# Performance work log

Hardware: AMD Instinct MI355X
Metric: run time of the kernel (lower is better)

## Reference

```python
import jax, jax.numpy as jnp
import numpy as np

N = 20000          # total atoms
NPG = 40           # atoms per molecule
G = N // NPG       # 500 graphs
DEG = 16           # neighbors per atom
E = N * DEG        # 320000 edges
HID = 128
NF = 128           # num_filters == num Gaussians
CUTOFF = 10.0
L = 3
IN_DIM = 100
LOG2 = 0.6931471805599453


def ssp(x):
    # ShiftedSoftplus: softplus(x) - log(2)
    return jax.nn.softplus(x) - LOG2


def setup_inputs() -> dict:
    key = jax.random.key(0)
    ks = jax.random.split(key, 16)
    rng = np.random.default_rng(0)

    # within-graph random edges, no self loops (mimics radius_graph structure)
    src = np.repeat(np.arange(N), DEG)
    base = (src // NPG) * NPG
    dst = base + (src - base + 1 + rng.integers(0, NPG - 1, size=E)) % NPG
    edge_index = jnp.asarray(np.stack([src, dst]).astype(np.int32))

    box = CUTOFF / np.sqrt(3.0)  # all pairwise distances < cutoff
    pos = jax.random.uniform(ks[0], (N, 3), dtype=jnp.float32) * box
    z = jax.random.randint(ks[1], (N,), 0, IN_DIM, dtype=jnp.int32)
    batch = jnp.asarray((np.arange(N) // NPG).astype(np.int32))

    s = 0.05
    emb = jax.random.normal(ks[2], (IN_DIM, HID), dtype=jnp.float32) * s
    mlp_w1 = jax.random.normal(ks[3], (L, NF, NF), dtype=jnp.float32) * s
    mlp_b1 = jnp.zeros((L, NF), jnp.float32)
    mlp_w2 = jax.random.normal(ks[4], (L, NF, NF), dtype=jnp.float32) * s
    mlp_b2 = jnp.zeros((L, NF), jnp.float32)
    cf_w1 = jax.random.normal(ks[5], (L, HID, NF), dtype=jnp.float32) * s   # no bias
    cf_w2 = jax.random.normal(ks[6], (L, NF, HID), dtype=jnp.float32) * s
    cf_b2 = jnp.zeros((L, HID), jnp.float32)
    lin_w = jax.random.normal(ks[7], (L, HID, HID), dtype=jnp.float32) * s
    lin_b = jnp.zeros((L, HID), jnp.float32)
    head_w1 = jax.random.normal(ks[8], (HID, HID // 2), dtype=jnp.float32) * s
    head_b1 = jnp.zeros((HID // 2,), jnp.float32)
    head_w2 = jax.random.normal(ks[9], (HID // 2, 1), dtype=jnp.float32) * s
    head_b2 = jnp.zeros((1,), jnp.float32)

    return dict(pos=pos, emb=emb, mlp_w1=mlp_w1, mlp_b1=mlp_b1, mlp_w2=mlp_w2,
                mlp_b2=mlp_b2, cf_w1=cf_w1, cf_w2=cf_w2, cf_b2=cf_b2,
                lin_w=lin_w, lin_b=lin_b, head_w1=head_w1, head_b1=head_b1,
                head_w2=head_w2, head_b2=head_b2, z=z, batch=batch,
                edge_index=edge_index)


def reference(pos, emb, mlp_w1, mlp_b1, mlp_w2, mlp_b2, cf_w1, cf_w2, cf_b2,
              lin_w, lin_b, head_w1, head_b1, head_w2, head_b2,
              z, batch, edge_index):
    row, col = edge_index[0], edge_index[1]  # source j, target i (PyG flow)
    d = jnp.linalg.norm(pos[row] - pos[col], axis=-1)  # [E]

    # Gaussian smearing
    offset = jnp.linspace(0.0, CUTOFF, NF)
    coeff = -0.5 / (offset[1] - offset[0]) ** 2
    edge_attr = jnp.exp(coeff * (d[:, None] - offset) ** 2)  # [E, NF]

    # cosine cutoff
    C = 0.5 * (jnp.cos(d * jnp.pi / CUTOFF) + 1.0)  # [E]

    h = emb[z]  # [N, HID]
    for l in range(L):
        # edge filter MLP
        Wf = ssp(edge_attr @ mlp_w1[l] + mlp_b1[l]) @ mlp_w2[l] + mlp_b2[l]
        Wf = Wf * C[:, None]                       # [E, NF]
        x1 = h @ cf_w1[l]                          # [N, NF]
        msg = x1[row] * Wf                         # gather + per-edge filter
        agg = jax.ops.segment_sum(msg, col, num_segments=N)  # scatter-add
        x = ssp(agg @ cf_w2[l] + cf_b2[l])
        x = x @ lin_w[l] + lin_b[l]
        h = h + x

    y = ssp(h @ head_w1 + head_b1) @ head_w2 + head_b2   # [N, 1]
    out = jax.ops.segment_sum(y, batch, num_segments=G).squeeze(-1)  # [G]
    return out
```

## Files before the change

kernel.cpp:

```cpp
#include <hip/hip_runtime.h>
#include <math.h>

#define N_ATOMS 20000
#define G_GRAPHS 500
#define NPG 40
#define DEG 16
#define E_EDGES (N_ATOMS * DEG)
#define EPM (NPG * DEG)
#define HID 128
#define NF 128
#define TBL2 80
#define TROWS (TBL2 + 2)
#define PROWS 81
#define CUTOFF 10.0f
#define LOG2F_ 0.6931471805599453f

typedef __attribute__((ext_vector_type(8))) short short8v;
typedef __attribute__((ext_vector_type(4))) float f32x4;
typedef __attribute__((ext_vector_type(2))) __bf16 bf16x2;
typedef unsigned short ushort_t;

__device__ __forceinline__ float ssp_f(float x) {
  float ax = fabsf(x);
  return fmaxf(x, 0.0f) + log1pf(expf(-ax)) - LOG2F_;
}
__device__ __forceinline__ ushort_t bf16rne(float x) {
  unsigned u = __float_as_uint(x);
  unsigned r = 0x7FFFu + ((u >> 16) & 1u);
  return (ushort_t)((u + r) >> 16);
}
__device__ __forceinline__ unsigned pk2(float a, float b) {
  return (unsigned)bf16rne(a) | ((unsigned)bf16rne(b) << 16);
}
__device__ __forceinline__ float bflo(unsigned u) { return __uint_as_float(u << 16); }
__device__ __forceinline__ float bfhi(unsigned u) { return __uint_as_float(u & 0xFFFF0000u); }
__device__ __forceinline__ int bidx(int row, int col) {
  return row * 128 + (col ^ ((row & 7) << 3));
}
__device__ __forceinline__ float fdot2b(unsigned a, unsigned b, float c) {
#if defined(__has_builtin) && __has_builtin(__builtin_amdgcn_fdot2_f32_bf16)
  return __builtin_amdgcn_fdot2_f32_bf16(__builtin_bit_cast(bf16x2, a),
                                         __builtin_bit_cast(bf16x2, b), c, false);
#else
  return fmaf(bflo(a), bflo(b), fmaf(bfhi(a), bfhi(b), c));
#endif
}

__global__ void k_table(const float* __restrict__ w1_, const float* __restrict__ b1_,
                        const float* __restrict__ w2_, const float* __restrict__ b2_,
                        ushort_t* __restrict__ table_) {
  __shared__ float eaT[NF][8];
  __shared__ float hvT[NF][8];
  int l = blockIdx.y;
  const float* w1 = w1_ + (size_t)l * NF * NF;
  const float* b1 = b1_ + (size_t)l * NF;
  const float* w2 = w2_ + (size_t)l * NF * NF;
  const float* b2 = b2_ + (size_t)l * NF;
  ushort_t* table = table_ + (size_t)l * TROWS * NF;
  int j = threadIdx.x;
  int rbase = blockIdx.x * 8;
  const float hh = CUTOFF / (float)(TBL2 - 1);
  const float delta = CUTOFF / (float)(NF - 1);
  const float coeff = -0.5f / (delta * delta);
#pragma unroll
  for (int rr = 0; rr < 8; ++rr) {
    float d = ((float)(rbase + rr) - 1.0f) * hh;
    float tt = d - delta * (float)j;
    eaT[j][rr] = expf(coeff * tt * tt);
  }
  __syncthreads();
  float acc[8], wreg[16];
  float b1j = b1[j];
#pragma unroll
  for (int rr = 0; rr < 8; ++rr) acc[rr] = b1j;
  for (int kb = 0; kb < NF; kb += 16) {
#pragma unroll
    for (int i = 0; i < 16; ++i) wreg[i] = w1[(kb + i) * NF + j];
#pragma unroll
    for (int i = 0; i < 16; ++i) {
      float4 e0 = *(const float4*)&eaT[kb + i][0];
      float4 e1 = *(const float4*)&eaT[kb + i][4];
      float wv = wreg[i];
      acc[0] = fmaf(e0.x, wv, acc[0]); acc[1] = fmaf(e0.y, wv, acc[1]);
      acc[2] = fmaf(e0.z, wv, acc[2]); acc[3] = fmaf(e0.w, wv, acc[3]);
      acc[4] = fmaf(e1.x, wv, acc[4]); acc[5] = fmaf(e1.y, wv, acc[5]);
      acc[6] = fmaf(e1.z, wv, acc[6]); acc[7] = fmaf(e1.w, wv, acc[7]);
    }
  }
#pragma unroll
  for (int rr = 0; rr < 8; ++rr) hvT[j][rr] = ssp_f(acc[rr]);
  __syncthreads();
  float b2j = b2[j];
#pragma unroll
  for (int rr = 0; rr < 8; ++rr) acc[rr] = b2j;
  for (int kb = 0; kb < NF; kb += 16) {
#pragma unroll
    for (int i = 0; i < 16; ++i) wreg[i] = w2[(kb + i) * NF + j];
#pragma unroll
    for (int i = 0; i < 16; ++i) {
      float4 e0 = *(const float4*)&hvT[kb + i][0];
      float4 e1 = *(const float4*)&hvT[kb + i][4];
      float wv = wreg[i];
      acc[0] = fmaf(e0.x, wv, acc[0]); acc[1] = fmaf(e0.y, wv, acc[1]);
      acc[2] = fmaf(e0.z, wv, acc[2]); acc[3] = fmaf(e0.w, wv, acc[3]);
      acc[4] = fmaf(e1.x, wv, acc[4]); acc[5] = fmaf(e1.y, wv, acc[5]);
      acc[6] = fmaf(e1.z, wv, acc[6]); acc[7] = fmaf(e1.w, wv, acc[7]);
    }
  }
#pragma unroll
  for (int rr = 0; rr < 8; ++rr) {
    int s = rbase + rr;
    if (s < TROWS) {
      float d = ((float)s - 1.0f) * hh;
      float C = 0.5f * (cosf(d * (float)M_PI / CUTOFF) + 1.0f);
      table[(size_t)s * NF + j] = bf16rne(acc[rr] * C);
    }
  }
}

__global__ void k_prep(const float* __restrict__ cf_w1, const float* __restrict__ cf_w2,
                       const float* __restrict__ lin_w, const float* __restrict__ hw1,
                       ushort_t* __restrict__ wtb) {
  __shared__ float tile[32][33];
  int b = blockIdx.x;
  int t = threadIdx.x;
  int tr = t >> 5, tc = t & 31;
  if (b < 36) {
    int m = b >> 2, tj = b & 3;
    int l = m / 3, ty = m % 3;
    const float* src = (ty == 0 ? cf_w1 : ty == 1 ? cf_w2 : lin_w) + (size_t)l * 128 * 128;
    ushort_t* dst = wtb + (size_t)m * 128 * 128;
    for (int ti = 0; ti < 4; ++ti) {
      __syncthreads();
#pragma unroll
      for (int i = 0; i < 4; ++i) {
        int r = tr + i * 8;
        tile[r][tc] = src[(ti * 32 + r) * 128 + tj * 32 + tc];
      }
      __syncthreads();
#pragma unroll
      for (int i = 0; i < 4; ++i) {
        int r = tr + i * 8;
        dst[(tj * 32 + r) * 128 + ti * 32 + tc] = bf16rne(tile[tc][r]);
      }
    }
  } else {
    int tj = b - 36;
    ushort_t* dst = wtb + (size_t)9 * 128 * 128;
    for (int ti = 0; ti < 4; ++ti) {
      __syncthreads();
#pragma unroll
      for (int i = 0; i < 4; ++i) {
        int r = tr + i * 8;
        tile[r][tc] = hw1[(ti * 32 + r) * 64 + tj * 32 + tc];
      }
      __syncthreads();
#pragma unroll
      for (int i = 0; i < 4; ++i) {
        int r = tr + i * 8;
        dst[(tj * 32 + r) * 128 + ti * 32 + tc] = bf16rne(tile[tc][r]);
      }
    }
  }
}

__global__ void __launch_bounds__(512) k_csr(const float* __restrict__ pos,
                                             const int* __restrict__ ei,
                                             uint4* __restrict__ ge,
                                             int* __restrict__ gstart) {
  __shared__ float spos[NPG * 3];
  __shared__ int cnt[NPG];
  __shared__ int pfx[NPG + 1];
  __shared__ uint4 epk[EPM];
  __shared__ unsigned char ecol[EPM];
  __shared__ short ssidx[EPM];
  int g = blockIdx.x, a0 = g * NPG, t = threadIdx.x;
  if (t < NPG * 3) spos[t] = pos[a0 * 3 + t];
  if (t < NPG) cnt[t] = 0;
  __syncthreads();
  int ebase = a0 * DEG;
  const float tscale = (float)(TBL2 - 1) / CUTOFF;
  for (int i = t; i < EPM; i += 512) {
    int r = ei[ebase + i] - a0;
    int c = ei[E_EDGES + ebase + i] - a0;
    float dx = spos[3 * r + 0] - spos[3 * c + 0];
    float dy = spos[3 * r + 1] - spos[3 * c + 1];
    float dz = spos[3 * r + 2] - spos[3 * c + 2];
    float ft = sqrtf(dx * dx + dy * dy + dz * dz) * tscale;
    int i0 = min((int)ft, TBL2 - 2);
    float tt = ft - (float)i0;
    float t2 = tt * tt, t3 = t2 * tt;
    float w0 = 0.5f * (-t3 + 2.f * t2 - tt);
    float w1 = 0.5f * (3.f * t3 - 5.f * t2 + 2.f);
    float w2 = 0.5f * (-3.f * t3 + 4.f * t2 + tt);
    float w3 = 0.5f * (t3 - t2);
    epk[i] = make_uint4(pk2(w0, w1), pk2(w2, w3), (unsigned)(i0 << 7),
                        (unsigned)((r << 6) | (((r & 7) << 2) << 16)));
    ecol[i] = (unsigned char)c;
    atomicAdd(&cnt[c], 1);
  }
  __syncthreads();
  if (t == 0) {
    int s = 0;
    for (int a = 0; a < NPG; ++a) { pfx[a] = s; s += cnt[a]; }
    pfx[NPG] = s;
  }
  __syncthreads();
  int w = t >> 6, lane = t & 63;
  for (int a = w * 5; a < w * 5 + 5; ++a) {
    int p = pfx[a];
#pragma unroll
    for (int ch = 0; ch < EPM / 64; ++ch) {
      int e = ch * 64 + lane;
      bool match = ((int)ecol[e] == a);
      unsigned long long bal = __ballot(match);
      if (match) ssidx[p + __popcll(bal & ((1ull << lane) - 1ull))] = (short)e;
      p += __popcll(bal);
    }
  }
  __syncthreads();
  for (int i = t; i < EPM; i += 512) ge[(size_t)g * EPM + i] = epk[ssidx[i]];
  if (t < NPG) gstart[g * NPG + t] = pfx[t];
}

__global__ void __launch_bounds__(512) k_mol(
    const float* __restrict__ emb, const int* __restrict__ z,
    const uint4* __restrict__ ge, const int* __restrict__ gstart,
    const ushort_t* __restrict__ tblb, const ushort_t* __restrict__ wtb,
    const float* __restrict__ cf_b2, const float* __restrict__ lin_b,
    const float* __restrict__ hb1, const float* __restrict__ hw2,
    const float* __restrict__ hb2, float* __restrict__ out) {
  __shared__ unsigned ptab[PROWS * 128];
  __shared__ ushort_t sb0[48 * 128];
  __shared__ ushort_t sb1[48 * 128];
  __shared__ uint4 sedge[EPM];
  __shared__ int sstart[NPG + 1];
  __shared__ float shead[48];
  __shared__ int sz[NPG];
  int g = blockIdx.x, a0 = g * NPG, t = threadIdx.x;
  int w = t >> 6, l6 = t & 63, r15 = l6 & 15, q = l6 >> 4;
  int colo = w * 16 + r15;
  int half = l6 >> 5, li = l6 & 31, ch0 = li * 4;

  {
    if (t < NPG) sz[t] = z[a0 + t];
    const uint4* gsrc = ge + (size_t)g * EPM;
    for (int i = t; i < EPM; i += 512) sedge[i] = gsrc[i];
    if (t < NPG) sstart[t] = gstart[g * NPG + t];
    if (t == 0) sstart[NPG] = EPM;
    if (t < 48) shead[t] = 0.f;
    ((unsigned*)sb0)[40 * 64 + t] = 0u;
    ((unsigned*)sb1)[40 * 64 + t] = 0u;
    const ushort_t* tg = tblb;
    for (int i = t; i < PROWS * 32; i += 512) {
      int s = i >> 5, c4 = (i & 31) << 2;
      uint2 ar = *(const uint2*)(tg + s * 128 + c4);
      uint2 br = *(const uint2*)(tg + (s + 1) * 128 + c4);
      uint4 o;
      o.x = (ar.x & 0xffffu) | (br.x << 16);
      o.y = (ar.x >> 16) | (br.x & 0xffff0000u);
      o.z = (ar.y & 0xffffu) | (br.y << 16);
      o.w = (ar.y >> 16) | (br.y & 0xffff0000u);
      *(uint4*)&ptab[(s << 7) + c4] = o;
    }
  }
  __syncthreads();

  float hreg[12];
#pragma unroll
  for (int mt = 0; mt < 3; ++mt) {
#pragma unroll
    for (int r = 0; r < 4; ++r) {
      int row = mt * 16 + q * 4 + r;
      float v = 0.f;
      if (row < NPG) {
        v = emb[(size_t)sz[row] * HID + colo];
        sb0[bidx(row, colo)] = bf16rne(v);
      }
      hreg[mt * 4 + r] = v;
    }
  }
  __syncthreads();

  for (int l = 0; l < 3; ++l) {
    const ushort_t* w1t = wtb + (size_t)(l * 3 + 0) * 128 * 128;
    const ushort_t* w2t = wtb + (size_t)(l * 3 + 1) * 128 * 128;
    const ushort_t* lwt = wtb + (size_t)(l * 3 + 2) * 128 * 128;
    if (l > 0) {
      const ushort_t* tg = tblb + (size_t)l * TROWS * 128;
      for (int i = t; i < PROWS * 32; i += 512) {
        int s = i >> 5, c4 = (i & 31) << 2;
        uint2 ar = *(const uint2*)(tg + s * 128 + c4);
        uint2 br = *(const uint2*)(tg + (s + 1) * 128 + c4);
        uint4 o;
        o.x = (ar.x & 0xffffu) | (br.x << 16);
        o.y = (ar.x >> 16) | (br.x & 0xffff0000u);
        o.z = (ar.y & 0xffffu) | (br.y << 16);
        o.w = (ar.y >> 16) | (br.y & 0xffff0000u);
        *(uint4*)&ptab[(s << 7) + c4] = o;
      }
    }
    {
      short8v bfr[4];
      const ushort_t* wp = w1t + (size_t)colo * 128 + q * 8;
#pragma unroll
      for (int ks = 0; ks < 4; ++ks) bfr[ks] = *(const short8v*)(wp + ks * 32);
#pragma unroll
      for (int mt = 0; mt < 3; ++mt) {
        f32x4 acc = (f32x4){0.f, 0.f, 0.f, 0.f};
#pragma unroll
        for (int ks = 0; ks < 4; ++ks) {
          short8v af = *(const short8v*)&sb0[bidx(mt * 16 + r15, ks * 32 + q * 8)];
          acc = __builtin_amdgcn_mfma_f32_16x16x32_bf16(af, bfr[ks], acc, 0, 0, 0);
        }
#pragma unroll
        for (int r = 0; r < 4; ++r) sb1[bidx(mt * 16 + q * 4 + r, colo)] = bf16rne(acc[r]);
      }
    }
    __syncthreads();
    {
      const unsigned* b1u = (const unsigned*)sb1;
      unsigned* b0u = (unsigned*)sb0;
      for (int a = w; a < NPG; a += 8) {
        int kb = sstart[a], ke = sstart[a + 1];
        float a0c = 0.f, a1c = 0.f, a2c = 0.f, a3c = 0.f;
        for (int k = kb; k < ke; k += 2) {
          int idx = k + half;
          uint4 ev = sedge[min(idx, EPM - 1)];
          bool ok = idx < ke;
          unsigned w01 = ok ? ev.x : 0u;
          unsigned w23 = ok ? ev.y : 0u;
          const unsigned* tb = ptab + ev.z + ch0;
          uint4 pa = *(const uint4*)tb;
          uint4 pb = *(const uint4*)(tb + 256);
          uint2 xv = *(const uint2*)&b1u[(ev.w & 0xffffu) + ((li * 2) ^ (ev.w >> 16))];
          float f0 = fdot2b(w01, pa.x, 0.f); f0 = fdot2b(w23, pb.x, f0);
          float f1 = fdot2b(w01, pa.y, 0.f); f1 = fdot2b(w23, pb.y, f1);
          float f2 = fdot2b(w01, pa.z, 0.f); f2 = fdot2b(w23, pb.z, f2);
          float f3 = fdot2b(w01, pa.w, 0.f); f3 = fdot2b(w23, pb.w, f3);
          a0c = fmaf(bflo(xv.x), f0, a0c);
          a1c = fmaf(bfhi(xv.x), f1, a1c);
          a2c = fmaf(bflo(xv.y), f2, a2c);
          a3c = fmaf(bfhi(xv.y), f3, a3c);
        }
        a0c += __shfl_xor(a0c, 32);
        a1c += __shfl_xor(a1c, 32);
        a2c += __shfl_xor(a2c, 32);
        a3c += __shfl_xor(a3c, 32);
        if (half == 0) {
          uint2 o;
          o.x = pk2(a0c, a1c);
          o.y = pk2(a2c, a3c);
          *(uint2*)&b0u[(a << 6) + ((li * 2) ^ ((a & 7) << 2))] = o;
        }
      }
    }
    __syncthreads();
    {
      float bc = cf_b2[(size_t)l * HID + colo];
      short8v bfr[4];
      const ushort_t* wp = w2t + (size_t)colo * 128 + q * 8;
#pragma unroll
      for (int ks = 0; ks < 4; ++ks) bfr[ks] = *(const short8v*)(wp + ks * 32);
#pragma unroll
      for (int mt = 0; mt < 3; ++mt) {
        f32x4 acc = (f32x4){0.f, 0.f, 0.f, 0.f};
#pragma unroll
        for (int ks = 0; ks < 4; ++ks) {
          short8v af = *(const short8v*)&sb0[bidx(mt * 16 + r15, ks * 32 + q * 8)];
          acc = __builtin_amdgcn_mfma_f32_16x16x32_bf16(af, bfr[ks], acc, 0, 0, 0);
        }
#pragma unroll
        for (int r = 0; r < 4; ++r) {
          int row = mt * 16 + q * 4 + r;
          float v = (row < NPG) ? ssp_f(acc[r] + bc) : 0.f;
          sb1[bidx(row, colo)] = bf16rne(v);
        }
      }
    }
    __syncthreads();
    {
      float bc = lin_b[(size_t)l * HID + colo];
      short8v bfr[4];
      const ushort_t* wp = lwt + (size_t)colo * 128 + q * 8;
#pragma unroll
      for (int ks = 0; ks < 4; ++ks) bfr[ks] = *(const short8v*)(wp + ks * 32);
#pragma unroll
      for (int mt = 0; mt < 3; ++mt) {
        f32x4 acc = (f32x4){0.f, 0.f, 0.f, 0.f};
#pragma unroll
        for (int ks = 0; ks < 4; ++ks) {
          short8v af = *(const short8v*)&sb1[bidx(mt * 16 + r15, ks * 32 + q * 8)];
          acc = __builtin_amdgcn_mfma_f32_16x16x32_bf16(af, bfr[ks], acc, 0, 0, 0);
        }
#pragma unroll
        for (int r = 0; r < 4; ++r) {
          int row = mt * 16 + q * 4 + r;
          if (row < NPG) {
            float nh = hreg[mt * 4 + r] + acc[r] + bc;
            hreg[mt * 4 + r] = nh;
            sb0[bidx(row, colo)] = bf16rne(nh);
          }
        }
      }
    }
    __syncthreads();
  }

  {
    const ushort_t* h1t = wtb + (size_t)9 * 128 * 128;
    for (int tile = w; tile < 12; tile += 8) {
      int mt = tile >> 2, nt = tile & 3;
      int col = nt * 16 + r15;
      short8v bfr[4];
      const ushort_t* wp = h1t + (size_t)col * 128 + q * 8;
#pragma unroll
      for (int ks = 0; ks < 4; ++ks) bfr[ks] = *(const short8v*)(wp + ks * 32);
      f32x4 acc = (f32x4){0.f, 0.f, 0.f, 0.f};
#pragma unroll
      for (int ks = 0; ks < 4; ++ks) {
        short8v af = *(const short8v*)&sb0[bidx(mt * 16 + r15, ks * 32 + q * 8)];
        acc = __builtin_amdgcn_mfma_f32_16x16x32_bf16(af, bfr[ks], acc, 0, 0, 0);
      }
      float hb = hb1[col];
      float w2v = hw2[col];
#pragma unroll
      for (int r = 0; r < 4; ++r) {
        int row = mt * 16 + q * 4 + r;
        float y = ssp_f(acc[r] + hb) * w2v;
        y += __shfl_xor(y, 1);
        y += __shfl_xor(y, 2);
        y += __shfl_xor(y, 4);
        y += __shfl_xor(y, 8);
        if (r15 == 0 && row < NPG) atomicAdd(&shead[row], y);
      }
    }
  }
  __syncthreads();
  if (w == 0) {
    float v = (l6 < NPG) ? shead[l6] : 0.f;
#pragma unroll
    for (int off = 32; off; off >>= 1) v += __shfl_xor(v, off);
    if (l6 == 0) out[g] = v + (float)NPG * hb2[0];
  }
}

extern "C" void kernel_launch(void* const* d_in, const int* in_sizes, int n_in,
                              void* d_out, int out_size, void* d_ws, size_t ws_size,
                              hipStream_t stream) {
  const float* pos    = (const float*)d_in[0];
  const float* emb    = (const float*)d_in[1];
  const float* mlp_w1 = (const float*)d_in[2];
  const float* mlp_b1 = (const float*)d_in[3];
  const float* mlp_w2 = (const float*)d_in[4];
  const float* mlp_b2 = (const float*)d_in[5];
  const float* cf_w1  = (const float*)d_in[6];
  const float* cf_w2  = (const float*)d_in[7];
  const float* cf_b2  = (const float*)d_in[8];
  const float* lin_w  = (const float*)d_in[9];
  const float* lin_b  = (const float*)d_in[10];
  const float* hw1    = (const float*)d_in[11];
  const float* hb1    = (const float*)d_in[12];
  const float* hw2    = (const float*)d_in[13];
  const float* hb2    = (const float*)d_in[14];
  const int*   z      = (const int*)d_in[15];
  const int*   ei     = (const int*)d_in[17];

  char* wsb = (char*)d_ws;
  uint4*    ge     = (uint4*)wsb;
  int*      gstart = (int*)(wsb + 5120000);
  ushort_t* tblb   = (ushort_t*)(wsb + 5200000);
  ushort_t* wtb    = (ushort_t*)(wsb + 5262976);
  size_t need = 5262976 + 327680;
  if (ws_size < need) return;

  k_table<<<dim3((TROWS + 7) / 8, 3), NF, 0, stream>>>(mlp_w1, mlp_b1, mlp_w2, mlp_b2, tblb);
  k_prep<<<38, 256, 0, stream>>>(cf_w1, cf_w2, lin_w, hw1, wtb);
  k_csr<<<G_GRAPHS, 512, 0, stream>>>(pos, ei, ge, gstart);
  k_mol<<<G_GRAPHS, 512, 0, stream>>>(emb, z, ge, gstart, tblb, wtb,
                                      cf_b2, lin_b, hb1, hw2, hb2, (float*)d_out);
}
```

Measured before the change: 113.4 us.

## Merge table, weight-prep and CSR kernels into one launch; pre-pair table rows

Fuses the three preprocessing kernels (filter table, weight transpose, per-graph CSR build) into a single launch that dispatches on block index, cutting two kernel launches and their serialization gaps. The filter table is now written in the paired-row layout k_mol consumes, so k_mol copies it into shared memory with plain uint4 loads instead of repacking two rows per layer. Per-atom edge lists are padded to even length with zero-weight edges, which removes the bounds check and select from the inner gather loop. Side effects are slightly more edge storage and idle threads in the table and transpose blocks of the merged launch.

```diff
diff --git a/kernel.cpp b/kernel.cpp
--- a/kernel.cpp
+++ b/kernel.cpp
@@ -7,6 +7,7 @@
 #define DEG 16
 #define E_EDGES (N_ATOMS * DEG)
 #define EPM (NPG * DEG)
+#define EPAD 680
 #define HID 128
 #define NF 128
 #define TBL2 80
@@ -46,194 +47,218 @@
 #endif
 }
 
-__global__ void k_table(const float* __restrict__ w1_, const float* __restrict__ b1_,
-                        const float* __restrict__ w2_, const float* __restrict__ b2_,
-                        ushort_t* __restrict__ table_) {
-  __shared__ float eaT[NF][8];
-  __shared__ float hvT[NF][8];
-  int l = blockIdx.y;
-  const float* w1 = w1_ + (size_t)l * NF * NF;
-  const float* b1 = b1_ + (size_t)l * NF;
-  const float* w2 = w2_ + (size_t)l * NF * NF;
-  const float* b2 = b2_ + (size_t)l * NF;
-  ushort_t* table = table_ + (size_t)l * TROWS * NF;
-  int j = threadIdx.x;
-  int rbase = blockIdx.x * 8;
-  const float hh = CUTOFF / (float)(TBL2 - 1);
-  const float delta = CUTOFF / (float)(NF - 1);
-  const float coeff = -0.5f / (delta * delta);
-#pragma unroll
-  for (int rr = 0; rr < 8; ++rr) {
-    float d = ((float)(rbase + rr) - 1.0f) * hh;
-    float tt = d - delta * (float)j;
-    eaT[j][rr] = expf(coeff * tt * tt);
-  }
-  __syncthreads();
-  float acc[8], wreg[16];
-  float b1j = b1[j];
-#pragma unroll
-  for (int rr = 0; rr < 8; ++rr) acc[rr] = b1j;
-  for (int kb = 0; kb < NF; kb += 16) {
-#pragma unroll
-    for (int i = 0; i < 16; ++i) wreg[i] = w1[(kb + i) * NF + j];
-#pragma unroll
-    for (int i = 0; i < 16; ++i) {
-      float4 e0 = *(const float4*)&eaT[kb + i][0];
-      float4 e1 = *(const float4*)&eaT[kb + i][4];
-      float wv = wreg[i];
-      acc[0] = fmaf(e0.x, wv, acc[0]); acc[1] = fmaf(e0.y, wv, acc[1]);
-      acc[2] = fmaf(e0.z, wv, acc[2]); acc[3] = fmaf(e0.w, wv, acc[3]);
-      acc[4] = fmaf(e1.x, wv, acc[4]); acc[5] = fmaf(e1.y, wv, acc[5]);
-      acc[6] = fmaf(e1.z, wv, acc[6]); acc[7] = fmaf(e1.w, wv, acc[7]);
-    }
-  }
-#pragma unroll
-  for (int rr = 0; rr < 8; ++rr) hvT[j][rr] = ssp_f(acc[rr]);
-  __syncthreads();
-  float b2j = b2[j];
-#pragma unroll
-  for (int rr = 0; rr < 8; ++rr) acc[rr] = b2j;
-  for (int kb = 0; kb < NF; kb += 16) {
-#pragma unroll
-    for (int i = 0; i < 16; ++i) wreg[i] = w2[(kb + i) * NF + j];
-#pragma unroll
-    for (int i = 0; i < 16; ++i) {
-      float4 e0 = *(const float4*)&hvT[kb + i][0];
-      float4 e1 = *(const float4*)&hvT[kb + i][4];
-      float wv = wreg[i];
-      acc[0] = fmaf(e0.x, wv, acc[0]); acc[1] = fmaf(e0.y, wv, acc[1]);
-      acc[2] = fmaf(e0.z, wv, acc[2]); acc[3] = fmaf(e0.w, wv, acc[3]);
-      acc[4] = fmaf(e1.x, wv, acc[4]); acc[5] = fmaf(e1.y, wv, acc[5]);
-      acc[6] = fmaf(e1.z, wv, acc[6]); acc[7] = fmaf(e1.w, wv, acc[7]);
-    }
-  }
-#pragma unroll
-  for (int rr = 0; rr < 8; ++rr) {
-    int s = rbase + rr;
-    if (s < TROWS) {
-      float d = ((float)s - 1.0f) * hh;
-      float C = 0.5f * (cosf(d * (float)M_PI / CUTOFF) + 1.0f);
-      table[(size_t)s * NF + j] = bf16rne(acc[rr] * C);
-    }
-  }
-}
-
-__global__ void k_prep(const float* __restrict__ cf_w1, const float* __restrict__ cf_w2,
-                       const float* __restrict__ lin_w, const float* __restrict__ hw1,
-                       ushort_t* __restrict__ wtb) {
-  __shared__ float tile[32][33];
+__global__ void __launch_bounds__(512) k_pre(
+    const float* __restrict__ mlp_w1, const float* __restrict__ mlp_b1,
+    const float* __restrict__ mlp_w2, const float* __restrict__ mlp_b2,
+    const float* __restrict__ cf_w1, const float* __restrict__ cf_w2,
+    const float* __restrict__ lin_w, const float* __restrict__ hw1,
+    const float* __restrict__ pos, const int* __restrict__ ei,
+    unsigned* __restrict__ ptabg, ushort_t* __restrict__ wtb,
+    uint4* __restrict__ ge, int* __restrict__ gstart) {
   int b = blockIdx.x;
   int t = threadIdx.x;
-  int tr = t >> 5, tc = t & 31;
-  if (b < 36) {
-    int m = b >> 2, tj = b & 3;
-    int l = m / 3, ty = m % 3;
-    const float* src = (ty == 0 ? cf_w1 : ty == 1 ? cf_w2 : lin_w) + (size_t)l * 128 * 128;
-    ushort_t* dst = wtb + (size_t)m * 128 * 128;
-    for (int ti = 0; ti < 4; ++ti) {
-      __syncthreads();
-#pragma unroll
-      for (int i = 0; i < 4; ++i) {
-        int r = tr + i * 8;
-        tile[r][tc] = src[(ti * 32 + r) * 128 + tj * 32 + tc];
-      }
-      __syncthreads();
-#pragma unroll
-      for (int i = 0; i < 4; ++i) {
-        int r = tr + i * 8;
-        dst[(tj * 32 + r) * 128 + ti * 32 + tc] = bf16rne(tile[tc][r]);
+
+  if (b < 33) {
+    __shared__ float eaT[NF][8];
+    __shared__ float hvT[NF][8];
+    int l = b / 11;
+    int rbase = (b % 11) * 8;
+    const float* w1 = mlp_w1 + (size_t)l * NF * NF;
+    const float* b1 = mlp_b1 + (size_t)l * NF;
+    const float* w2 = mlp_w2 + (size_t)l * NF * NF;
+    const float* b2 = mlp_b2 + (size_t)l * NF;
+    ushort_t* pp = (ushort_t*)(ptabg + (size_t)l * PROWS * 128);
+    const float hh = CUTOFF / (float)(TBL2 - 1);
+    const float delta = CUTOFF / (float)(NF - 1);
+    const float coeff = -0.5f / (delta * delta);
+    int j = t & 127;
+    bool act = t < 128;
+    if (act) {
+#pragma unroll
+      for (int rr = 0; rr < 8; ++rr) {
+        float d = ((float)(rbase + rr) - 1.0f) * hh;
+        float tt = d - delta * (float)j;
+        eaT[j][rr] = expf(coeff * tt * tt);
+      }
+    }
+    __syncthreads();
+    float acc[8], wreg[16];
+    if (act) {
+      float b1j = b1[j];
+#pragma unroll
+      for (int rr = 0; rr < 8; ++rr) acc[rr] = b1j;
+      for (int kb = 0; kb < NF; kb += 16) {
+#pragma unroll
+        for (int i = 0; i < 16; ++i) wreg[i] = w1[(kb + i) * NF + j];
+#pragma unroll
+        for (int i = 0; i < 16; ++i) {
+          float4 e0 = *(const float4*)&eaT[kb + i][0];
+          float4 e1 = *(const float4*)&eaT[kb + i][4];
+          float wv = wreg[i];
+          acc[0] = fmaf(e0.x, wv, acc[0]); acc[1] = fmaf(e0.y, wv, acc[1]);
+          acc[2] = fmaf(e0.z, wv, acc[2]); acc[3] = fmaf(e0.w, wv, acc[3]);
+          acc[4] = fmaf(e1.x, wv, acc[4]); acc[5] = fmaf(e1.y, wv, acc[5]);
+          acc[6] = fmaf(e1.z, wv, acc[6]); acc[7] = fmaf(e1.w, wv, acc[7]);
+        }
+      }
+#pragma unroll
+      for (int rr = 0; rr < 8; ++rr) hvT[j][rr] = ssp_f(acc[rr]);
+    }
+    __syncthreads();
+    if (act) {
+      float b2j = b2[j];
+#pragma unroll
+      for (int rr = 0; rr < 8; ++rr) acc[rr] = b2j;
+      for (int kb = 0; kb < NF; kb += 16) {
+#pragma unroll
+        for (int i = 0; i < 16; ++i) wreg[i] = w2[(kb + i) * NF + j];
+#pragma unroll
+        for (int i = 0; i < 16; ++i) {
+          float4 e0 = *(const float4*)&hvT[kb + i][0];
+          float4 e1 = *(const float4*)&hvT[kb + i][4];
+          float wv = wreg[i];
+          acc[0] = fmaf(e0.x, wv, acc[0]); acc[1] = fmaf(e0.y, wv, acc[1]);
+          acc[2] = fmaf(e0.z, wv, acc[2]); acc[3] = fmaf(e0.w, wv, acc[3]);
+          acc[4] = fmaf(e1.x, wv, acc[4]); acc[5] = fmaf(e1.y, wv, acc[5]);
+          acc[6] = fmaf(e1.z, wv, acc[6]); acc[7] = fmaf(e1.w, wv, acc[7]);
+        }
+      }
+#pragma unroll
+      for (int rr = 0; rr < 8; ++rr) {
+        int s = rbase + rr;
+        if (s < TROWS) {
+          float d = ((float)s - 1.0f) * hh;
+          float C = 0.5f * (cosf(d * (float)M_PI / CUTOFF) + 1.0f);
+          ushort_t v = bf16rne(acc[rr] * C);
+          if (s < PROWS) pp[(s * 128 + j) * 2] = v;
+          if (s >= 1) pp[((s - 1) * 128 + j) * 2 + 1] = v;
+        }
+      }
+    }
+  } else if (b < 71) {
+    __shared__ float tile[32][33];
+    int pb = b - 33;
+    int tr = (t & 255) >> 5, tc = t & 31;
+    bool act = t < 256;
+    if (pb < 36) {
+      int m = pb >> 2, tj = pb & 3;
+      int l = m / 3, ty = m % 3;
+      const float* src = (ty == 0 ? cf_w1 : ty == 1 ? cf_w2 : lin_w) + (size_t)l * 128 * 128;
+      ushort_t* dst = wtb + (size_t)m * 128 * 128;
+      for (int ti = 0; ti < 4; ++ti) {
+        __syncthreads();
+        if (act) {
+#pragma unroll
+          for (int i = 0; i < 4; ++i) {
+            int r = tr + i * 8;
+            tile[r][tc] = src[(ti * 32 + r) * 128 + tj * 32 + tc];
+          }
+        }
+        __syncthreads();
+        if (act) {
+#pragma unroll
+          for (int i = 0; i < 4; ++i) {
+            int r = tr + i * 8;
+            dst[(tj * 32 + r) * 128 + ti * 32 + tc] = bf16rne(tile[tc][r]);
+          }
+        }
+      }
+    } else {
+      int tj = pb - 36;
+      ushort_t* dst = wtb + (size_t)9 * 128 * 128;
+      for (int ti = 0; ti < 4; ++ti) {
+        __syncthreads();
+        if (act) {
+#pragma unroll
+          for (int i = 0; i < 4; ++i) {
+            int r = tr + i * 8;
+            tile[r][tc] = hw1[(ti * 32 + r) * 64 + tj * 32 + tc];
+          }
+        }
+        __syncthreads();
+        if (act) {
+#pragma unroll
+          for (int i = 0; i < 4; ++i) {
+            int r = tr + i * 8;
+            dst[(tj * 32 + r) * 128 + ti * 32 + tc] = bf16rne(tile[tc][r]);
+          }
+        }
       }
     }
   } else {
-    int tj = b - 36;
-    ushort_t* dst = wtb + (size_t)9 * 128 * 128;
-    for (int ti = 0; ti < 4; ++ti) {
-      __syncthreads();
-#pragma unroll
-      for (int i = 0; i < 4; ++i) {
-        int r = tr + i * 8;
-        tile[r][tc] = hw1[(ti * 32 + r) * 64 + tj * 32 + tc];
-      }
-      __syncthreads();
-#pragma unroll
-      for (int i = 0; i < 4; ++i) {
-        int r = tr + i * 8;
-        dst[(tj * 32 + r) * 128 + ti * 32 + tc] = bf16rne(tile[tc][r]);
-      }
-    }
-  }
-}
-
-__global__ void __launch_bounds__(512) k_csr(const float* __restrict__ pos,
-                                             const int* __restrict__ ei,
-                                             uint4* __restrict__ ge,
-                                             int* __restrict__ gstart) {
-  __shared__ float spos[NPG * 3];
-  __shared__ int cnt[NPG];
-  __shared__ int pfx[NPG + 1];
-  __shared__ uint4 epk[EPM];
-  __shared__ unsigned char ecol[EPM];
-  __shared__ short ssidx[EPM];
-  int g = blockIdx.x, a0 = g * NPG, t = threadIdx.x;
-  if (t < NPG * 3) spos[t] = pos[a0 * 3 + t];
-  if (t < NPG) cnt[t] = 0;
-  __syncthreads();
-  int ebase = a0 * DEG;
-  const float tscale = (float)(TBL2 - 1) / CUTOFF;
-  for (int i = t; i < EPM; i += 512) {
-    int r = ei[ebase + i] - a0;
-    int c = ei[E_EDGES + ebase + i] - a0;
-    float dx = spos[3 * r + 0] - spos[3 * c + 0];
-    float dy = spos[3 * r + 1] - spos[3 * c + 1];
-    float dz = spos[3 * r + 2] - spos[3 * c + 2];
-    float ft = sqrtf(dx * dx + dy * dy + dz * dz) * tscale;
-    int i0 = min((int)ft, TBL2 - 2);
-    float tt = ft - (float)i0;
-    float t2 = tt * tt, t3 = t2 * tt;
-    float w0 = 0.5f * (-t3 + 2.f * t2 - tt);
-    float w1 = 0.5f * (3.f * t3 - 5.f * t2 + 2.f);
-    float w2 = 0.5f * (-3.f * t3 + 4.f * t2 + tt);
-    float w3 = 0.5f * (t3 - t2);
-    epk[i] = make_uint4(pk2(w0, w1), pk2(w2, w3), (unsigned)(i0 << 7),
-                        (unsigned)((r << 6) | (((r & 7) << 2) << 16)));
-    ecol[i] = (unsigned char)c;
-    atomicAdd(&cnt[c], 1);
-  }
-  __syncthreads();
-  if (t == 0) {
-    int s = 0;
-    for (int a = 0; a < NPG; ++a) { pfx[a] = s; s += cnt[a]; }
-    pfx[NPG] = s;
-  }
-  __syncthreads();
-  int w = t >> 6, lane = t & 63;
-  for (int a = w * 5; a < w * 5 + 5; ++a) {
-    int p = pfx[a];
-#pragma unroll
-    for (int ch = 0; ch < EPM / 64; ++ch) {
-      int e = ch * 64 + lane;
-      bool match = ((int)ecol[e] == a);
-      unsigned long long bal = __ballot(match);
-      if (match) ssidx[p + __popcll(bal & ((1ull << lane) - 1ull))] = (short)e;
-      p += __popcll(bal);
-    }
-  }
-  __syncthreads();
-  for (int i = t; i < EPM; i += 512) ge[(size_t)g * EPM + i] = epk[ssidx[i]];
-  if (t < NPG) gstart[g * NPG + t] = pfx[t];
+    __shared__ float spos[NPG * 3];
+    __shared__ int cnt[NPG];
+    __shared__ int pfx[NPG + 1];
+    __shared__ uint4 epk[EPM];
+    __shared__ unsigned char ecol[EPM];
+    __shared__ short ssidx[EPAD];
+    int g = b - 71, a0 = g * NPG;
+    if (t < NPG * 3) spos[t] = pos[a0 * 3 + t];
+    if (t < NPG) cnt[t] = 0;
+    for (int i = t; i < EPAD; i += 512) ssidx[i] = -1;
+    __syncthreads();
+    int ebase = a0 * DEG;
+    const float tscale = (float)(TBL2 - 1) / CUTOFF;
+    for (int i = t; i < EPM; i += 512) {
+      int r = ei[ebase + i] - a0;
+      int c = ei[E_EDGES + ebase + i] - a0;
+      float dx = spos[3 * r + 0] - spos[3 * c + 0];
+      float dy = spos[3 * r + 1] - spos[3 * c + 1];
+      float dz = spos[3 * r + 2] - spos[3 * c + 2];
+      float ft = sqrtf(dx * dx + dy * dy + dz * dz) * tscale;
+      int i0 = min((int)ft, TBL2 - 2);
+      float tt = ft - (float)i0;
+      float t2 = tt * tt, t3 = t2 * tt;
+      float w0 = 0.5f * (-t3 + 2.f * t2 - tt);
+      float w1 = 0.5f * (3.f * t3 - 5.f * t2 + 2.f);
+      float w2 = 0.5f * (-3.f * t3 + 4.f * t2 + tt);
+      float w3 = 0.5f * (t3 - t2);
+      epk[i] = make_uint4(pk2(w0, w1), pk2(w2, w3), (unsigned)(i0 << 7),
+                          (unsigned)((r << 6) | (((r & 7) << 2) << 16)));
+      ecol[i] = (unsigned char)c;
+      atomicAdd(&cnt[c], 1);
+    }
+    __syncthreads();
+    if (t == 0) {
+      int s = 0;
+      for (int a = 0; a < NPG; ++a) { pfx[a] = s; s += (cnt[a] + 1) & ~1; }
+      pfx[NPG] = s;
+    }
+    __syncthreads();
+    int w = t >> 6, lane = t & 63;
+    for (int a = w * 5; a < w * 5 + 5; ++a) {
+      int p = pfx[a];
+#pragma unroll
+      for (int ch = 0; ch < EPM / 64; ++ch) {
+        int e = ch * 64 + lane;
+        bool match = ((int)ecol[e] == a);
+        unsigned long long bal = __ballot(match);
+        if (match) ssidx[p + __popcll(bal & ((1ull << lane) - 1ull))] = (short)e;
+        p += __popcll(bal);
+      }
+    }
+    __syncthreads();
+    int ptot = pfx[NPG];
+    const uint4 z4 = make_uint4(0u, 0u, 0u, 0u);
+    for (int i = t; i < ptot; i += 512) {
+      int e = ssidx[i];
+      ge[(size_t)g * EPAD + i] = (e >= 0) ? epk[e] : z4;
+    }
+    if (t <= NPG) gstart[g * (NPG + 1) + t] = pfx[t];
+  }
 }
 
 __global__ void __launch_bounds__(512) k_mol(
     const float* __restrict__ emb, const int* __restrict__ z,
     const uint4* __restrict__ ge, const int* __restrict__ gstart,
-    const ushort_t* __restrict__ tblb, const ushort_t* __restrict__ wtb,
+    const unsigned* __restrict__ ptabg, const ushort_t* __restrict__ wtb,
     const float* __restrict__ cf_b2, const float* __restrict__ lin_b,
     const float* __restrict__ hb1, const float* __restrict__ hw2,
     const float* __restrict__ hb2, float* __restrict__ out) {
   __shared__ unsigned ptab[PROWS * 128];
   __shared__ ushort_t sb0[48 * 128];
   __shared__ ushort_t sb1[48 * 128];
-  __shared__ uint4 sedge[EPM];
+  __shared__ uint4 sedge[EPAD];
   __shared__ int sstart[NPG + 1];
   __shared__ float shead[48];
   __shared__ int sz[NPG];
@@ -242,27 +267,18 @@
   int colo = w * 16 + r15;
   int half = l6 >> 5, li = l6 & 31, ch0 = li * 4;
 
+  int ptot = gstart[g * (NPG + 1) + NPG];
   {
     if (t < NPG) sz[t] = z[a0 + t];
-    const uint4* gsrc = ge + (size_t)g * EPM;
-    for (int i = t; i < EPM; i += 512) sedge[i] = gsrc[i];
-    if (t < NPG) sstart[t] = gstart[g * NPG + t];
-    if (t == 0) sstart[NPG] = EPM;
+    if (t <= NPG) sstart[t] = gstart[g * (NPG + 1) + t];
+    const uint4* gsrc = ge + (size_t)g * EPAD;
+    for (int i = t; i < ptot; i += 512) sedge[i] = gsrc[i];
     if (t < 48) shead[t] = 0.f;
     ((unsigned*)sb0)[40 * 64 + t] = 0u;
     ((unsigned*)sb1)[40 * 64 + t] = 0u;
-    const ushort_t* tg = tblb;
-    for (int i = t; i < PROWS * 32; i += 512) {
-      int s = i >> 5, c4 = (i & 31) << 2;
-      uint2 ar = *(const uint2*)(tg + s * 128 + c4);
-      uint2 br = *(const uint2*)(tg + (s + 1) * 128 + c4);
-      uint4 o;
-      o.x = (ar.x & 0xffffu) | (br.x << 16);
-      o.y = (ar.x >> 16) | (br.x & 0xffff0000u);
-      o.z = (ar.y & 0xffffu) | (br.y << 16);
-      o.w = (ar.y >> 16) | (br.y & 0xffff0000u);
-      *(uint4*)&ptab[(s << 7) + c4] = o;
-    }
+    const uint4* tg4 = (const uint4*)ptabg;
+    uint4* st4 = (uint4*)ptab;
+    for (int i = t; i < PROWS * 32; i += 512) st4[i] = tg4[i];
   }
   __syncthreads();
 
@@ -287,18 +303,9 @@
     const ushort_t* w2t = wtb + (size_t)(l * 3 + 1) * 128 * 128;
     const ushort_t* lwt = wtb + (size_t)(l * 3 + 2) * 128 * 128;
     if (l > 0) {
-      const ushort_t* tg = tblb + (size_t)l * TROWS * 128;
-      for (int i = t; i < PROWS * 32; i += 512) {
-        int s = i >> 5, c4 = (i & 31) << 2;
-        uint2 ar = *(const uint2*)(tg + s * 128 + c4);
-        uint2 br = *(const uint2*)(tg + (s + 1) * 128 + c4);
-        uint4 o;
-        o.x = (ar.x & 0xffffu) | (br.x << 16);
-        o.y = (ar.x >> 16) | (br.x & 0xffff0000u);
-        o.z = (ar.y & 0xffffu) | (br.y << 16);
-        o.w = (ar.y >> 16) | (br.y & 0xffff0000u);
-        *(uint4*)&ptab[(s << 7) + c4] = o;
-      }
+      const uint4* tg4 = (const uint4*)(ptabg + (size_t)l * PROWS * 128);
+      uint4* st4 = (uint4*)ptab;
+      for (int i = t; i < PROWS * 32; i += 512) st4[i] = tg4[i];
     }
     {
       short8v bfr[4];
@@ -324,20 +331,16 @@
       for (int a = w; a < NPG; a += 8) {
         int kb = sstart[a], ke = sstart[a + 1];
         float a0c = 0.f, a1c = 0.f, a2c = 0.f, a3c = 0.f;
-        for (int k = kb; k < ke; k += 2) {
-          int idx = k + half;
-          uint4 ev = sedge[min(idx, EPM - 1)];
-          bool ok = idx < ke;
-          unsigned w01 = ok ? ev.x : 0u;
-          unsigned w23 = ok ? ev.y : 0u;
+        for (int k = kb + half; k < ke; k += 2) {
+          uint4 ev = sedge[k];
           const unsigned* tb = ptab + ev.z + ch0;
           uint4 pa = *(const uint4*)tb;
           uint4 pb = *(const uint4*)(tb + 256);
           uint2 xv = *(const uint2*)&b1u[(ev.w & 0xffffu) + ((li * 2) ^ (ev.w >> 16))];
-          float f0 = fdot2b(w01, pa.x, 0.f); f0 = fdot2b(w23, pb.x, f0);
-          float f1 = fdot2b(w01, pa.y, 0.f); f1 = fdot2b(w23, pb.y, f1);
-          float f2 = fdot2b(w01, pa.z, 0.f); f2 = fdot2b(w23, pb.z, f2);
-          float f3 = fdot2b(w01, pa.w, 0.f); f3 = fdot2b(w23, pb.w, f3);
+          float f0 = fdot2b(ev.x, pa.x, 0.f); f0 = fdot2b(ev.y, pb.x, f0);
+          float f1 = fdot2b(ev.x, pa.y, 0.f); f1 = fdot2b(ev.y, pb.y, f1);
+          float f2 = fdot2b(ev.x, pa.z, 0.f); f2 = fdot2b(ev.y, pb.z, f2);
+          float f3 = fdot2b(ev.x, pa.w, 0.f); f3 = fdot2b(ev.y, pb.w, f3);
           a0c = fmaf(bflo(xv.x), f0, a0c);
           a1c = fmaf(bfhi(xv.x), f1, a1c);
           a2c = fmaf(bflo(xv.y), f2, a2c);
@@ -468,15 +471,14 @@
 
   char* wsb = (char*)d_ws;
   uint4*    ge     = (uint4*)wsb;
-  int*      gstart = (int*)(wsb + 5120000);
-  ushort_t* tblb   = (ushort_t*)(wsb + 5200000);
-  ushort_t* wtb    = (ushort_t*)(wsb + 5262976);
-  size_t need = 5262976 + 327680;
+  int*      gstart = (int*)(wsb + 5440000);
+  unsigned* ptabg  = (unsigned*)(wsb + 5522000);
+  ushort_t* wtb    = (ushort_t*)(wsb + 5646416);
+  size_t need = 5646416 + 327680;
   if (ws_size < need) return;
 
-  k_table<<<dim3((TROWS + 7) / 8, 3), NF, 0, stream>>>(mlp_w1, mlp_b1, mlp_w2, mlp_b2, tblb);
-  k_prep<<<38, 256, 0, stream>>>(cf_w1, cf_w2, lin_w, hw1, wtb);
-  k_csr<<<G_GRAPHS, 512, 0, stream>>>(pos, ei, ge, gstart);
-  k_mol<<<G_GRAPHS, 512, 0, stream>>>(emb, z, ge, gstart, tblb, wtb,
+  k_pre<<<571, 512, 0, stream>>>(mlp_w1, mlp_b1, mlp_w2, mlp_b2, cf_w1, cf_w2, lin_w,
+                                 hw1, pos, ei, ptabg, wtb, ge, gstart);
+  k_mol<<<G_GRAPHS, 512, 0, stream>>>(emb, z, ge, gstart, ptabg, wtb,
                                       cf_b2, lin_b, hb1, hw2, hb2, (float*)d_out);
 }
```

Measured after the change: 104.9 us. 1.08x faster.
